# Optimization experiments

Measured on AMD Instinct MI355X. Metric: run time of the kernel, lower is better.

Reference implementation:

```python
import jax, jax.numpy as jnp
import numpy as np

L, B, S, D, H, F = 3, 2, 2048, 256, 8, 1024
DK = D // H
EPS = 1e-7


def _positional_encoding(max_len: int, dim: int) -> jnp.ndarray:
    # pos in [1, max_len], i in [1, dim]; w = pos / 10000**((2*i//2)/dim) == pos / 10000**(i/dim)
    pos = np.arange(1, max_len + 1, dtype=np.float64)[:, None]
    i = np.arange(1, dim + 1)
    w = pos / np.power(10000.0, i.astype(np.float64) / dim)[None, :]
    pe = np.where((i % 2 == 0)[None, :], np.sin(w), np.cos(w))
    return jnp.asarray(pe, jnp.float32)


def _ln(x, g, b):
    mu = jnp.mean(x, axis=-1, keepdims=True)
    var = jnp.mean((x - mu) ** 2, axis=-1, keepdims=True)
    return (x - mu) / jnp.sqrt(var + EPS) * g + b


def setup_inputs() -> dict:
    key = jax.random.key(0)
    ks = jax.random.split(key, 16)
    s = 0.05
    inp = {
        "x": jax.random.normal(ks[0], (B, S, D), jnp.float32),
        "mask": jax.random.randint(ks[1], (B, S, S), 0, 2).astype(bool),
        "pe": _positional_encoding(S, D),
        "Wq": jax.random.normal(ks[2], (L, H, D, DK), jnp.float32) * s,
        "Wk": jax.random.normal(ks[3], (L, H, D, DK), jnp.float32) * s,
        "Wv": jax.random.normal(ks[4], (L, H, D, DK), jnp.float32) * s,
        "Wo": jax.random.normal(ks[5], (L, D, D), jnp.float32) * s,
        "bo": jnp.zeros((L, D), jnp.float32),
        "ln1_g": jnp.ones((L, D), jnp.float32),
        "ln1_b": jnp.zeros((L, D), jnp.float32),
        "W1": jax.random.normal(ks[6], (L, D, F), jnp.float32) * s,
        "b1": jnp.zeros((L, F), jnp.float32),
        "W2": jax.random.normal(ks[7], (L, F, D), jnp.float32) * s,
        "b2": jnp.zeros((L, D), jnp.float32),
        "ln2_g": jnp.ones((L, D), jnp.float32),
        "ln2_b": jnp.zeros((L, D), jnp.float32),
    }
    return inp


def _encoder_layer(x, mask, Wq, Wk, Wv, Wo, bo, ln1_g, ln1_b, W1, b1, W2, b2, ln2_g, ln2_b):
    # all heads batched: [B,S,D] x [H,D,dk] -> [B,H,S,dk]
    q = jnp.einsum('bsd,hdk->bhsk', x, Wq)
    k = jnp.einsum('bsd,hdk->bhsk', x, Wk)
    v = jnp.einsum('bsd,hdk->bhsk', x, Wv)
    scores = jnp.einsum('bhsk,bhtk->bhst', q, k) / jnp.sqrt(jnp.float32(DK))
    neg = -jnp.finfo(jnp.float32).max
    scores = jnp.where(mask[:, None, :, :], neg, scores)
    attn = jax.nn.softmax(scores, axis=-1)
    # concat heads along feature dim (head-major order as torch.cat dim=2)
    o = jnp.einsum('bhst,bhtv->bshv', attn, v).reshape(x.shape[0], x.shape[1], D)
    o = o @ Wo + bo
    x = _ln(o + x, ln1_g, ln1_b)  # post-norm (prenorm=False), dropout_rate=0
    h = jax.nn.relu(x @ W1 + b1) @ W2 + b2
    x = _ln(h + x, ln2_g, ln2_b)
    return x


def reference(x, mask, pe, Wq, Wk, Wv, Wo, bo, ln1_g, ln1_b, W1, b1, W2, b2, ln2_g, ln2_b):
    x = x + pe[None, : x.shape[1], :]
    for l in range(L):
        x = _encoder_layer(x, mask, Wq[l], Wk[l], Wv[l], Wo[l], bo[l], ln1_g[l], ln1_b[l],
                           W1[l], b1[l], W2[l], b2[l], ln2_g[l], ln2_b[l])
    return x
```

## Files before the change

### kernel.cpp

```cpp
#include <hip/hip_runtime.h>
#include <hip/hip_bf16.h>
#include <cfloat>

#define Lc 3
#define Bc 2
#define Sc 2048
#define Dc 256
#define Hc 8
#define DKc 32
#define Fc 1024

typedef __hip_bfloat16 bf16;
typedef short s8v __attribute__((ext_vector_type(8)));
typedef float f4v __attribute__((ext_vector_type(4)));

#define QSCALE 0.25504526036067815f

#if __has_builtin(__builtin_amdgcn_exp2f)
#define EXP2(x) __builtin_amdgcn_exp2f(x)
#else
#define EXP2(x) exp2f(x)
#endif

__device__ __forceinline__ float load_f(const void* p, size_t i, int isbf)
{
    return isbf ? __bfloat162float(((const bf16*)p)[i]) : ((const float*)p)[i];
}

typedef const __attribute__((address_space(1))) char gchar_t;
typedef __attribute__((address_space(3))) char lchar_t;
__device__ __forceinline__ void glds16(const void* g, void* l)
{
    __builtin_amdgcn_global_load_lds((gchar_t*)(size_t)g, (lchar_t*)(size_t)l,
                                     16, 0, 0);
}

#define NBLK_REPACK 2304
#define NBLK_CONV   6942
#define NBLK_PACK   1024
#define NBLK_PE     4096

__global__ __launch_bounds__(256) void prologue_fused(
    const void* __restrict__ x, const void* __restrict__ mask,
    const void* __restrict__ pe,
    const void* Wq, const void* Wk, const void* Wv,
    const void* Wo, const void* W1, const void* W2,
    const void* bo, const void* b1, const void* b2,
    const void* g1, const void* be1, const void* g2, const void* be2,
    bf16* __restrict__ wqkv, bf16* __restrict__ dstb, float* __restrict__ pc,
    unsigned* __restrict__ pmask, float* __restrict__ xf,
    bf16* __restrict__ xb, int* __restrict__ flags)
{
    __shared__ int sf[2];
    int tid = threadIdx.x;
    if (tid < 64) {
        const unsigned short* u16 = (const unsigned short*)x;
        int cnt = 0;
        for (int i = tid; i < 256; i += 64) {
            unsigned e = (u16[2 * i] >> 7) & 0xFF;
            cnt += (e >= 90 && e <= 140) ? 1 : 0;
        }
        #pragma unroll
        for (int d = 1; d < 64; d <<= 1) cnt += __shfl_xor(cnt, d);
        const unsigned* mu = (const unsigned*)mask;
        int c2 = ((mu[tid] & 0xFFFFFF00u) == 0) ? 1 : 0;
        #pragma unroll
        for (int d = 1; d < 64; d <<= 1) c2 += __shfl_xor(c2, d);
        if (tid == 0) {
            sf[0] = (cnt >= 128) ? 1 : 0;
            sf[1] = (c2 >= 48) ? 1 : 0;
            if (blockIdx.x == 0) { flags[0] = sf[0]; flags[1] = sf[1]; }
        }
    }
    __syncthreads();
    int isbf = sf[0], mf = sf[1];
    int blk = blockIdx.x;

    if (blk < NBLK_REPACK) {
        int idx = blk * 256 + tid;
        int l   = idx / (3 * Dc * Dc);
        int rem = idx % (3 * Dc * Dc);
        int col = rem / Dc;
        int d   = rem % Dc;
        int mat = col / Dc;
        int hk  = col % Dc;
        int h = hk / DKc, kk = hk % DKc;
        const void* W = (mat == 0) ? Wq : (mat == 1) ? Wk : Wv;
        float v = load_f(W, (size_t)l * (Hc * Dc * DKc) + h * (Dc * DKc) + d * DKc + kk, isbf);
        wqkv[idx] = __float2bfloat16(v);
    } else if (blk < NBLK_REPACK + NBLK_CONV) {
        const int NB0 = Lc * Dc * Dc;
        const int NB1 = NB0 + Lc * Dc * Fc;
        const int NB2 = NB1 + Lc * Fc * Dc;
        int idx = (blk - NBLK_REPACK) * 256 + tid;
        if (idx < NB2) {
            const void* src; int off;
            if (idx < NB0) {
                int l = idx / (Dc * Dc); int rem = idx % (Dc * Dc);
                int n = rem / Dc, k = rem % Dc;
                src = Wo; off = l * Dc * Dc + k * Dc + n;
            } else if (idx < NB1) {
                int j = idx - NB0;
                int l = j / (Fc * Dc); int rem = j % (Fc * Dc);
                int n = rem / Dc, k = rem % Dc;
                src = W1; off = l * Dc * Fc + k * Fc + n;
            } else {
                int j = idx - NB1;
                int l = j / (Dc * Fc); int rem = j % (Dc * Fc);
                int n = rem / Fc, k = rem % Fc;
                src = W2; off = l * Fc * Dc + k * Dc + n;
            }
            dstb[idx] = __float2bfloat16(load_f(src, off, isbf));
        } else {
            int off = idx - NB2;
            if (off < 7680) {
                const void* src; int lo;
                if (off < 768)       { src = bo;  lo = off; }
                else if (off < 3840) { src = b1;  lo = off - 768; }
                else if (off < 4608) { src = b2;  lo = off - 3840; }
                else if (off < 5376) { src = g1;  lo = off - 4608; }
                else if (off < 6144) { src = be1; lo = off - 5376; }
                else if (off < 6912) { src = g2;  lo = off - 6144; }
                else                 { src = be2; lo = off - 6912; }
                pc[off] = load_f(src, lo, isbf);
            }
        }
    } else if (blk < NBLK_REPACK + NBLK_CONV + NBLK_PACK) {
        int idx = (blk - NBLK_REPACK - NBLK_CONV) * 256 + tid;
        unsigned wb = 0;
        if (mf) {
            const int* mp = (const int*)mask + (size_t)idx * 32;
            #pragma unroll
            for (int u = 0; u < 8; ++u) {
                uint4 q = *(const uint4*)(mp + u * 4);
                wb |= (q.x ? 1u : 0u) << (u * 4);
                wb |= (q.y ? 1u : 0u) << (u * 4 + 1);
                wb |= (q.z ? 1u : 0u) << (u * 4 + 2);
                wb |= (q.w ? 1u : 0u) << (u * 4 + 3);
            }
        } else {
            const unsigned char* mp = (const unsigned char*)mask + (size_t)idx * 32;
            uint4 a = *(const uint4*)mp;
            uint4 bq = *(const uint4*)(mp + 16);
            const unsigned char* ab = (const unsigned char*)&a;
            const unsigned char* bb = (const unsigned char*)&bq;
            #pragma unroll
            for (int j = 0; j < 16; ++j) {
                wb |= (ab[j] ? 1u : 0u) << j;
                wb |= (bb[j] ? 1u : 0u) << (16 + j);
            }
        }
        pmask[idx] = wb;
    } else {
        int idx = (blk - NBLK_REPACK - NBLK_CONV - NBLK_PACK) * 256 + tid;
        int rem = idx % (Sc * Dc);
        float v = load_f(x, idx, isbf) + load_f(pe, rem, isbf);
        xf[idx] = v;
        xb[idx] = __float2bfloat16(v);
    }
}

__global__ __launch_bounds__(256) void gemm_mfma(
    const bf16* __restrict__ A, const bf16* __restrict__ BT,
    const float* __restrict__ bias, void* __restrict__ C,
    bf16* __restrict__ vt,
    int M, int N, int K, int relu, int obf, float ascale, int scale_ncols,
    int ldc)
{
    __shared__ __align__(16) short As[4096];
    __shared__ __align__(16) short Bs[4096];
    int tid = threadIdx.x;
    int w = tid >> 6, lane = tid & 63;
    int quad = lane >> 4, l15 = lane & 15;
    int wm0 = (w & 1) * 32, wn0 = (w >> 1) * 32;
    int row0 = blockIdx.y * 64, col0 = blockIdx.x * 64;

    int s0 = w * 128 + lane;
    int s1 = s0 + 64;
    int r0 = s0 >> 3, c0 = ((s0 & 7) ^ (r0 & 7)) * 8;
    int r1 = s1 >> 3, c1 = ((s1 & 7) ^ (r1 & 7)) * 8;
    const bf16* Ag0 = A + (size_t)(row0 + r0) * K + c0;
    const bf16* Ag1 = A + (size_t)(row0 + r1) * K + c1;
    const bf16* Bg0 = BT + (size_t)(col0 + r0) * K + c0;
    const bf16* Bg1 = BT + (size_t)(col0 + r1) * K + c1;
    short* Ad0 = As + w * 1024;
    short* Ad1 = As + w * 1024 + 512;
    short* Bd0 = Bs + w * 1024;
    short* Bd1 = Bs + w * 1024 + 512;

    f4v acc00 = {0.f,0.f,0.f,0.f}, acc01 = acc00, acc10 = acc00, acc11 = acc00;

    int m0 = wm0 + l15, m1 = wm0 + 16 + l15;
    int n0 = wn0 + l15, n1 = wn0 + 16 + l15;
    int sw7 = l15 & 7;

    for (int k0 = 0; k0 < K; k0 += 64) {
        glds16(Ag0 + k0, Ad0);
        glds16(Ag1 + k0, Ad1);
        glds16(Bg0 + k0, Bd0);
        glds16(Bg1 + k0, Bd1);
        __syncthreads();
        #pragma unroll
        for (int kc = 0; kc < 2; ++kc) {
            int sw = ((kc * 4 + quad) ^ sw7) * 8;
            s8v a0 = *(const s8v*)(As + m0 * 64 + sw);
            s8v a1 = *(const s8v*)(As + m1 * 64 + sw);
            s8v b0 = *(const s8v*)(Bs + n0 * 64 + sw);
            s8v b1 = *(const s8v*)(Bs + n1 * 64 + sw);
            acc00 = __builtin_amdgcn_mfma_f32_16x16x32_bf16(a0, b0, acc00, 0, 0, 0);
            acc01 = __builtin_amdgcn_mfma_f32_16x16x32_bf16(a0, b1, acc01, 0, 0, 0);
            acc10 = __builtin_amdgcn_mfma_f32_16x16x32_bf16(a1, b0, acc10, 0, 0, 0);
            acc11 = __builtin_amdgcn_mfma_f32_16x16x32_bf16(a1, b1, acc11, 0, 0, 0);
        }
        __syncthreads();
    }

    f4v accs[2][2] = {{acc00, acc01}, {acc10, acc11}};

    if (vt && col0 >= 2 * Dc) {
        #pragma unroll
        for (int mt = 0; mt < 2; ++mt) {
            #pragma unroll
            for (int nt = 0; nt < 2; ++nt) {
                int lc = wn0 + nt * 16 + l15;
                #pragma unroll
                for (int reg = 0; reg < 4; ++reg) {
                    int lr = wm0 + mt * 16 + quad * 4 + reg;
                    int p = ((lr & 15) << 2) | (lr >> 4);
                    bf16 bv = __float2bfloat16(accs[mt][nt][reg]);
                    As[lc * 64 + (p ^ ((lc & 7) << 3))] = *(short*)&bv;
                }
            }
        }
        __syncthreads();
        int bI = row0 >> 11;
        int srow = row0 & (Sc - 1);
        #pragma unroll
        for (int j = 0; j < 2; ++j) {
            int e = j * 256 + tid;
            int c = e >> 3, p0 = (e & 7) * 8;
            s8v vv = *(const s8v*)(As + c * 64 + (p0 ^ ((c & 7) << 3)));
            int gcv = col0 - 2 * Dc + c;
            size_t vb = ((size_t)(bI * Hc + (gcv >> 5)) * DKc + (gcv & 31)) * Sc
                        + srow + p0;
            *(s8v*)(vt + vb) = vv;
        }
        return;
    }

    float bv0 = bias ? bias[col0 + wn0 + l15] : 0.f;
    float bv1 = bias ? bias[col0 + wn0 + 16 + l15] : 0.f;
    #pragma unroll
    for (int mt = 0; mt < 2; ++mt) {
        #pragma unroll
        for (int nt = 0; nt < 2; ++nt) {
            int gr = row0 + wm0 + mt * 16 + quad * 4;
            int gc = col0 + wn0 + nt * 16 + l15;
            float badd = nt ? bv1 : bv0;
            float sc = (gc < scale_ncols) ? ascale : 1.f;
            #pragma unroll
            for (int reg = 0; reg < 4; ++reg) {
                float v = accs[mt][nt][reg] * sc + badd;
                if (relu) v = fmaxf(v, 0.f);
                if (obf) ((bf16*)C)[(size_t)(gr + reg) * ldc + gc] = __float2bfloat16(v);
                else     ((float*)C)[(size_t)(gr + reg) * ldc + gc] = v;
            }
        }
    }
}

__global__ __launch_bounds__(256) void gemm_mfma32(
    const bf16* __restrict__ A, const bf16* __restrict__ BT,
    const float* __restrict__ bias, void* __restrict__ C,
    int M, int N, int K, int relu, int obf)
{
    __shared__ __align__(16) short As[2048];
    __shared__ __align__(16) short Bs[4096];
    int tid = threadIdx.x;
    int w = tid >> 6, lane = tid & 63;
    int quad = lane >> 4, l15 = lane & 15;
    int wm0 = (w & 1) * 16, wn0 = (w >> 1) * 32;
    int row0 = blockIdx.y * 32, col0 = blockIdx.x * 64;

    int sa = w * 64 + lane;
    int ra = sa >> 3, ca = ((sa & 7) ^ (ra & 7)) * 8;
    int s0 = w * 128 + lane, s1 = s0 + 64;
    int r0 = s0 >> 3, c0 = ((s0 & 7) ^ (r0 & 7)) * 8;
    int r1 = s1 >> 3, c1 = ((s1 & 7) ^ (r1 & 7)) * 8;
    const bf16* Ag  = A + (size_t)(row0 + ra) * K + ca;
    const bf16* Bg0 = BT + (size_t)(col0 + r0) * K + c0;
    const bf16* Bg1 = BT + (size_t)(col0 + r1) * K + c1;
    short* Ad  = As + w * 512;
    short* Bd0 = Bs + w * 1024;
    short* Bd1 = Bs + w * 1024 + 512;

    f4v acc0 = {0.f,0.f,0.f,0.f}, acc1 = acc0;

    int m0 = wm0 + l15;
    int n0 = wn0 + l15, n1 = wn0 + 16 + l15;
    int sw7 = l15 & 7;

    for (int k0 = 0; k0 < K; k0 += 64) {
        glds16(Ag + k0, Ad);
        glds16(Bg0 + k0, Bd0);
        glds16(Bg1 + k0, Bd1);
        __syncthreads();
        #pragma unroll
        for (int kc = 0; kc < 2; ++kc) {
            int sw = ((kc * 4 + quad) ^ sw7) * 8;
            s8v a0 = *(const s8v*)(As + m0 * 64 + sw);
            s8v b0 = *(const s8v*)(Bs + n0 * 64 + sw);
            s8v b1 = *(const s8v*)(Bs + n1 * 64 + sw);
            acc0 = __builtin_amdgcn_mfma_f32_16x16x32_bf16(a0, b0, acc0, 0, 0, 0);
            acc1 = __builtin_amdgcn_mfma_f32_16x16x32_bf16(a0, b1, acc1, 0, 0, 0);
        }
        __syncthreads();
    }

    float bv0 = bias ? bias[col0 + wn0 + l15] : 0.f;
    float bv1 = bias ? bias[col0 + wn0 + 16 + l15] : 0.f;
    f4v accs[2] = {acc0, acc1};
    #pragma unroll
    for (int nt = 0; nt < 2; ++nt) {
        int gr = row0 + wm0 + quad * 4;
        int gc = col0 + wn0 + nt * 16 + l15;
        float badd = nt ? bv1 : bv0;
        #pragma unroll
        for (int reg = 0; reg < 4; ++reg) {
            float v = accs[nt][reg] + badd;
            if (relu) v = fmaxf(v, 0.f);
            if (obf) ((bf16*)C)[(size_t)(gr + reg) * N + gc] = __float2bfloat16(v);
            else     ((float*)C)[(size_t)(gr + reg) * N + gc] = v;
        }
    }
}

__global__ __launch_bounds__(256) void flash_mfma(
    const bf16* __restrict__ qkv, const bf16* __restrict__ vt,
    const unsigned* __restrict__ pmask,
    bf16* __restrict__ op0, bf16* __restrict__ op1,
    bf16* __restrict__ op2, bf16* __restrict__ op3,
    float* __restrict__ spart)
{
    __shared__ __align__(16) short Ks[2][2048];
    __shared__ __align__(16) short Vs[2][2048];
    __shared__ __align__(16) short Pw[4][16 * 72];

    int tid = threadIdx.x;
    int w = tid >> 6;
    int lane = tid & 63;
    int quad = lane >> 4, l15 = lane & 15;
    int q0 = blockIdx.x * 64;
    int h = blockIdx.y;
    int z = blockIdx.z;
    int b = z >> 2, rng = z & 3;
    bf16* op = (rng == 0) ? op0 : (rng == 1) ? op1 : (rng == 2) ? op2 : op3;

    s8v qfrag = *(const s8v*)(qkv + (size_t)(b * Sc + q0 + w * 16 + l15) * 512 + h * 32 + quad * 8);

    int sr = tid >> 3, ss = tid & 7;
    int c8 = ss ^ (sr & 7);
    const bf16* kg = qkv + (size_t)(b * Sc + rng * (Sc / 4) + 2 * sr + (c8 >> 2)) * 512
                     + 256 + h * 32 + (c8 & 3) * 8;
    const bf16* vg = vt + ((size_t)(b * Hc + h) * DKc + sr) * Sc + rng * (Sc / 4) + c8 * 8;

    int koff = (l15 >> 1) * 64 + ((((l15 & 1) << 2) + quad) ^ ((l15 >> 1) & 7)) * 8;
    int pfoff = l15 * 72 + quad * 8;
    int vkey = l15 & 7;
    int voff = l15 * 64;

    f4v o0 = {0.f,0.f,0.f,0.f}, o1 = o0;
    float ssum[4] = {0.f, 0.f, 0.f, 0.f};

    short* pwv = Pw[w];
    const unsigned* mp = pmask + (size_t)b * Sc * (Sc / 32)
                         + (size_t)(q0 + w * 16 + quad * 4) * (Sc / 32) + rng * 16;

#define FSTAGE(bi, it2) do { \
        glds16(kg + (size_t)(it2) * (64 * 512), Ks[bi] + w * 512); \
        glds16(vg + (it2) * 64, Vs[bi] + w * 512); \
    } while (0)

    FSTAGE(0, 0);
    for (int it = 0; it < 8; ++it) {
        int cur = it & 1;
        __syncthreads();
        if (it < 7) FSTAGE(cur ^ 1, it + 1);

        uint2 mw[4];
        #pragma unroll
        for (int reg = 0; reg < 4; ++reg)
            mw[reg] = *(const uint2*)(mp + reg * (Sc / 32) + it * 2);

        const short* kb = Ks[cur];
        f4v sfr[4];
        __builtin_amdgcn_s_setprio(1);
        #pragma unroll
        for (int nt = 0; nt < 4; ++nt) {
            s8v kf = *(const s8v*)(kb + koff + nt * 512);
            f4v zz = {0.f,0.f,0.f,0.f};
            sfr[nt] = __builtin_amdgcn_mfma_f32_16x16x32_bf16(qfrag, kf, zz, 0, 0, 0);
        }
        __builtin_amdgcn_s_setprio(0);
        #pragma unroll
        for (int reg = 0; reg < 4; ++reg) {
            unsigned ta = mw[reg].x >> l15;
            unsigned tb = mw[reg].y >> l15;
            float p0 = EXP2(sfr[0][reg]); if (ta & 1u)         p0 = 0.f;
            float p1 = EXP2(sfr[1][reg]); if ((ta >> 16) & 1u) p1 = 0.f;
            float p2 = EXP2(sfr[2][reg]); if (tb & 1u)         p2 = 0.f;
            float p3 = EXP2(sfr[3][reg]); if ((tb >> 16) & 1u) p3 = 0.f;
            ssum[reg] += (p0 + p1) + (p2 + p3);
            __hip_bfloat162 plo = __float22bfloat162_rn(make_float2(p0, p1));
            __hip_bfloat162 phi = __float22bfloat162_rn(make_float2(p2, p3));
            uint2 pk = {*(unsigned*)&plo, *(unsigned*)&phi};
            *(uint2*)(pwv + (quad * 4 + reg) * 72 + l15 * 4) = pk;
        }
        const short* vb = Vs[cur];
        __builtin_amdgcn_s_setprio(1);
        #pragma unroll
        for (int kc = 0; kc < 2; ++kc) {
            s8v pf = *(const s8v*)(pwv + pfoff + kc * 32);
            int vo = voff + (((kc * 4 + quad) ^ vkey) * 8);
            s8v vf0 = *(const s8v*)(vb + vo);
            s8v vf1 = *(const s8v*)(vb + vo + 1024);
            o0 = __builtin_amdgcn_mfma_f32_16x16x32_bf16(pf, vf0, o0, 0, 0, 0);
            o1 = __builtin_amdgcn_mfma_f32_16x16x32_bf16(pf, vf1, o1, 0, 0, 0);
        }
        __builtin_amdgcn_s_setprio(0);
    }
#undef FSTAGE

    #pragma unroll
    for (int reg = 0; reg < 4; ++reg) {
        #pragma unroll
        for (int d = 1; d < 16; d <<= 1) ssum[reg] += __shfl_xor(ssum[reg], d);
    }

    #pragma unroll
    for (int reg = 0; reg < 4; ++reg) {
        int row = q0 + w * 16 + quad * 4 + reg;
        size_t ob = (size_t)(b * Sc + row) * Dc + h * DKc;
        op[ob + l15]      = __float2bfloat16(o0[reg]);
        op[ob + 16 + l15] = __float2bfloat16(o1[reg]);
        if (l15 == 0)
            spart[((size_t)(rng * Bc + b) * Hc + h) * Sc + row] = ssum[reg];
    }
}

__global__ __launch_bounds__(256) void attn_merge(
    const bf16* __restrict__ op0, const bf16* __restrict__ op1,
    const bf16* __restrict__ op2, const bf16* __restrict__ op3,
    const float* __restrict__ spart, bf16* __restrict__ attn_out)
{
    int t8 = blockIdx.x * 256 + threadIdx.x;
    size_t idx = (size_t)t8 * 8;
    int d = (int)(idx & 255);
    int h = d >> 5;
    int row = (int)((idx >> 8) & (Sc - 1));
    int b = (int)(idx >> 19);
    float s = 0.f;
    #pragma unroll
    for (int r = 0; r < 4; ++r)
        s += spart[((size_t)(r * Bc + b) * Hc + h) * Sc + row];
    float inv = 1.f / fmaxf(s, 1e-30f);

    uint4 a0 = *(const uint4*)(op0 + idx);
    uint4 a1 = *(const uint4*)(op1 + idx);
    uint4 a2 = *(const uint4*)(op2 + idx);
    uint4 a3 = *(const uint4*)(op3 + idx);
    const unsigned short* u0 = (const unsigned short*)&a0;
    const unsigned short* u1 = (const unsigned short*)&a1;
    const unsigned short* u2 = (const unsigned short*)&a2;
    const unsigned short* u3 = (const unsigned short*)&a3;
    unsigned short outv[8];
    #pragma unroll
    for (int j = 0; j < 8; ++j) {
        float o = (__uint_as_float((unsigned)u0[j] << 16) + __uint_as_float((unsigned)u1[j] << 16))
                + (__uint_as_float((unsigned)u2[j] << 16) + __uint_as_float((unsigned)u3[j] << 16));
        bf16 ov = __float2bfloat16(o * inv);
        outv[j] = *(unsigned short*)&ov;
    }
    *(uint4*)(attn_out + idx) = *(uint4*)outv;
}

__global__ __launch_bounds__(256) void add_ln(
    const float* __restrict__ a, float* __restrict__ xf, bf16* __restrict__ xb,
    const float* __restrict__ g, const float* __restrict__ b,
    void* __restrict__ dout, const int* __restrict__ flags)
{
    __shared__ float ws4[2][4];
    int row = blockIdx.x, d = threadIdx.x;
    size_t idx = (size_t)row * Dc + d;
    float v = a[idx] + xf[idx];
    float s = v;
    #pragma unroll
    for (int dd = 1; dd < 64; dd <<= 1) s += __shfl_xor(s, dd);
    if ((d & 63) == 0) ws4[0][d >> 6] = s;
    __syncthreads();
    float mu = (ws4[0][0] + ws4[0][1] + ws4[0][2] + ws4[0][3]) * (1.f / Dc);
    float c = v - mu;
    float q = c * c;
    #pragma unroll
    for (int dd = 1; dd < 64; dd <<= 1) q += __shfl_xor(q, dd);
    if ((d & 63) == 0) ws4[1][d >> 6] = q;
    __syncthreads();
    float var = (ws4[1][0] + ws4[1][1] + ws4[1][2] + ws4[1][3]) * (1.f / Dc);
    float r2 = c * rsqrtf(var + 1e-7f) * g[d] + b[d];
    xf[idx] = r2;
    xb[idx] = __float2bfloat16(r2);
    if (dout) {
        if (flags[0]) ((bf16*)dout)[idx] = __float2bfloat16(r2);
        else          ((float*)dout)[idx] = r2;
    }
}

extern "C" void kernel_launch(void* const* d_in, const int* in_sizes, int n_in,
                              void* d_out, int out_size, void* d_ws, size_t ws_size,
                              hipStream_t stream)
{
    const void* x    = d_in[0];
    const void* mask = d_in[1];
    const void* pe   = d_in[2];
    const void* Wq   = d_in[3];
    const void* Wk   = d_in[4];
    const void* Wv   = d_in[5];
    const void* Wo   = d_in[6];
    const void* bo   = d_in[7];
    const void* ln1g = d_in[8];
    const void* ln1b = d_in[9];
    const void* W1   = d_in[10];
    const void* b1   = d_in[11];
    const void* W2   = d_in[12];
    const void* b2   = d_in[13];
    const void* ln2g = d_in[14];
    const void* ln2b = d_in[15];

    const int M = Bc * Sc;
    char* ws = (char*)d_ws;
    const size_t MB = 1024 * 1024;
    int*      flags    = (int*)ws;
    float*    xf32     = (float*)(ws + 256);
    float*    obuf     = (float*)(ws + 256 + 4 * MB);
    char*     bigc     = ws + 256 + 8 * MB;
    bf16*     xbf      = (bf16*)(ws + 256 + 16 * MB);
    bf16*     attn_out = (bf16*)(ws + 256 + 18 * MB);
    bf16*     wqkv     = (bf16*)(ws + 256 + 20 * MB);
    bf16*     woc      = wqkv + (size_t)Lc * Dc * 3 * Dc;
    bf16*     w1c      = woc + (size_t)Lc * Dc * Dc;
    bf16*     w2c      = w1c + (size_t)Lc * Dc * Fc;
    float*    pc       = (float*)(w2c + (size_t)Lc * Fc * Dc);
    unsigned* pmask    = (unsigned*)(ws + 256 + 25 * MB);
    float*    spart    = (float*)(ws + 256 + 26 * MB);

    bf16* qkv  = (bf16*)bigc;
    bf16* vtb  = (bf16*)(bigc + 4 * MB);
    bf16* hbuf = (bf16*)bigc;
    bf16* op0  = (bf16*)obuf;
    bf16* op1  = op0 + (size_t)M * Dc;
    bf16* op2  = attn_out;
    bf16* op3  = (bf16*)(bigc + 6 * MB);

    float* pc_bo   = pc;
    float* pc_b1   = pc + 768;
    float* pc_b2   = pc + 3840;
    float* pc_ln1g = pc + 4608;
    float* pc_ln1b = pc + 5376;
    float* pc_ln2g = pc + 6144;
    float* pc_ln2b = pc + 6912;

    prologue_fused<<<NBLK_REPACK + NBLK_CONV + NBLK_PACK + NBLK_PE, 256, 0, stream>>>(
        x, mask, pe, Wq, Wk, Wv, Wo, W1, W2, bo, b1, b2,
        ln1g, ln1b, ln2g, ln2b, wqkv, woc, pc, pmask, xf32, xbf, flags);

    for (int l = 0; l < Lc; ++l) {
        gemm_mfma<<<dim3(3 * Dc / 64, M / 64), 256, 0, stream>>>(
            xbf, wqkv + (size_t)l * Dc * 3 * Dc, nullptr, qkv, vtb,
            M, 3 * Dc, Dc, 0, 1, QSCALE, Dc, 512);
        flash_mfma<<<dim3(Sc / 64, Hc, Bc * 4), 256, 0, stream>>>(
            qkv, vtb, pmask, op0, op1, op2, op3, spart);
        attn_merge<<<(Bc * Sc * Dc / 8) / 256, 256, 0, stream>>>(
            op0, op1, op2, op3, spart, attn_out);
        gemm_mfma32<<<dim3(Dc / 64, M / 32), 256, 0, stream>>>(
            attn_out, woc + (size_t)l * Dc * Dc, pc_bo + l * Dc, obuf, M, Dc, Dc, 0, 0);
        add_ln<<<M, 256, 0, stream>>>(obuf, xf32, xbf,
            pc_ln1g + l * Dc, pc_ln1b + l * Dc, nullptr, flags);
        gemm_mfma<<<dim3(Fc / 64, M / 64), 256, 0, stream>>>(
            xbf, w1c + (size_t)l * Dc * Fc, pc_b1 + l * Fc, hbuf, nullptr,
            M, Fc, Dc, 1, 1, 1.f, 0, Fc);
        gemm_mfma32<<<dim3(Dc / 64, M / 32), 256, 0, stream>>>(
            hbuf, w2c + (size_t)l * Fc * Dc, pc_b2 + l * Dc, obuf, M, Dc, Fc, 0, 0);
        add_ln<<<M, 256, 0, stream>>>(obuf, xf32, xbf,
            pc_ln2g + l * Dc, pc_ln2b + l * Dc,
            (l == Lc - 1) ? d_out : nullptr, flags);
    }
}
```

Before: 356.0 us.

## Double-buffer LDS tiles in MFMA GEMM kernels to overlap loads with compute

Both GEMM kernels now keep two LDS buffers and issue the global-to-LDS loads for the next K tile before computing on the current one, using a single barrier per iteration instead of two. The aim is to hide global load latency behind the MFMA work and cut synchronisation. In exchange, LDS use per block doubles, which can lower occupancy. Correctness relies on the glds16 async writes being visible by the next barrier, and it is unclear whether that barrier waits on the outstanding vmcnt.

```diff
diff --git a/kernel.cpp b/kernel.cpp
--- a/kernel.cpp
+++ b/kernel.cpp
@@ -167,8 +167,8 @@
     int M, int N, int K, int relu, int obf, float ascale, int scale_ncols,
     int ldc)
 {
-    __shared__ __align__(16) short As[4096];
-    __shared__ __align__(16) short Bs[4096];
+    __shared__ __align__(16) short As[2][4096];
+    __shared__ __align__(16) short Bs[2][4096];
     int tid = threadIdx.x;
     int w = tid >> 6, lane = tid & 63;
     int quad = lane >> 4, l15 = lane & 15;
@@ -183,10 +183,6 @@
     const bf16* Ag1 = A + (size_t)(row0 + r1) * K + c1;
     const bf16* Bg0 = BT + (size_t)(col0 + r0) * K + c0;
     const bf16* Bg1 = BT + (size_t)(col0 + r1) * K + c1;
-    short* Ad0 = As + w * 1024;
-    short* Ad1 = As + w * 1024 + 512;
-    short* Bd0 = Bs + w * 1024;
-    short* Bd1 = Bs + w * 1024 + 512;
 
     f4v acc00 = {0.f,0.f,0.f,0.f}, acc01 = acc00, acc10 = acc00, acc11 = acc00;
 
@@ -194,30 +190,39 @@
     int n0 = wn0 + l15, n1 = wn0 + 16 + l15;
     int sw7 = l15 & 7;
 
+#define GSTAGE(bi, kk) do { \
+        glds16(Ag0 + (kk), As[bi] + w * 1024); \
+        glds16(Ag1 + (kk), As[bi] + w * 1024 + 512); \
+        glds16(Bg0 + (kk), Bs[bi] + w * 1024); \
+        glds16(Bg1 + (kk), Bs[bi] + w * 1024 + 512); \
+    } while (0)
+
+    GSTAGE(0, 0);
     for (int k0 = 0; k0 < K; k0 += 64) {
-        glds16(Ag0 + k0, Ad0);
-        glds16(Ag1 + k0, Ad1);
-        glds16(Bg0 + k0, Bd0);
-        glds16(Bg1 + k0, Bd1);
+        int cur = (k0 >> 6) & 1;
         __syncthreads();
+        if (k0 + 64 < K) GSTAGE(cur ^ 1, k0 + 64);
+        const short* Ab = As[cur];
+        const short* Bb = Bs[cur];
         #pragma unroll
         for (int kc = 0; kc < 2; ++kc) {
             int sw = ((kc * 4 + quad) ^ sw7) * 8;
-            s8v a0 = *(const s8v*)(As + m0 * 64 + sw);
-            s8v a1 = *(const s8v*)(As + m1 * 64 + sw);
-            s8v b0 = *(const s8v*)(Bs + n0 * 64 + sw);
-            s8v b1 = *(const s8v*)(Bs + n1 * 64 + sw);
+            s8v a0 = *(const s8v*)(Ab + m0 * 64 + sw);
+            s8v a1 = *(const s8v*)(Ab + m1 * 64 + sw);
+            s8v b0 = *(const s8v*)(Bb + n0 * 64 + sw);
+            s8v b1 = *(const s8v*)(Bb + n1 * 64 + sw);
             acc00 = __builtin_amdgcn_mfma_f32_16x16x32_bf16(a0, b0, acc00, 0, 0, 0);
             acc01 = __builtin_amdgcn_mfma_f32_16x16x32_bf16(a0, b1, acc01, 0, 0, 0);
             acc10 = __builtin_amdgcn_mfma_f32_16x16x32_bf16(a1, b0, acc10, 0, 0, 0);
             acc11 = __builtin_amdgcn_mfma_f32_16x16x32_bf16(a1, b1, acc11, 0, 0, 0);
         }
+    }
+#undef GSTAGE
+
+    f4v accs[2][2] = {{acc00, acc01}, {acc10, acc11}};
+
+    if (vt && col0 >= 2 * Dc) {
         __syncthreads();
-    }
-
-    f4v accs[2][2] = {{acc00, acc01}, {acc10, acc11}};
-
-    if (vt && col0 >= 2 * Dc) {
         #pragma unroll
         for (int mt = 0; mt < 2; ++mt) {
             #pragma unroll
@@ -228,7 +233,7 @@
                     int lr = wm0 + mt * 16 + quad * 4 + reg;
                     int p = ((lr & 15) << 2) | (lr >> 4);
                     bf16 bv = __float2bfloat16(accs[mt][nt][reg]);
-                    As[lc * 64 + (p ^ ((lc & 7) << 3))] = *(short*)&bv;
+                    As[0][lc * 64 + (p ^ ((lc & 7) << 3))] = *(short*)&bv;
                 }
             }
         }
@@ -239,7 +244,7 @@
         for (int j = 0; j < 2; ++j) {
             int e = j * 256 + tid;
             int c = e >> 3, p0 = (e & 7) * 8;
-            s8v vv = *(const s8v*)(As + c * 64 + (p0 ^ ((c & 7) << 3)));
+            s8v vv = *(const s8v*)(As[0] + c * 64 + (p0 ^ ((c & 7) << 3)));
             int gcv = col0 - 2 * Dc + c;
             size_t vb = ((size_t)(bI * Hc + (gcv >> 5)) * DKc + (gcv & 31)) * Sc
                         + srow + p0;
@@ -274,8 +279,8 @@
     const float* __restrict__ bias, void* __restrict__ C,
     int M, int N, int K, int relu, int obf)
 {
-    __shared__ __align__(16) short As[2048];
-    __shared__ __align__(16) short Bs[4096];
+    __shared__ __align__(16) short As[2][2048];
+    __shared__ __align__(16) short Bs[2][4096];
     int tid = threadIdx.x;
     int w = tid >> 6, lane = tid & 63;
     int quad = lane >> 4, l15 = lane & 15;
@@ -290,9 +295,6 @@
     const bf16* Ag  = A + (size_t)(row0 + ra) * K + ca;
     const bf16* Bg0 = BT + (size_t)(col0 + r0) * K + c0;
     const bf16* Bg1 = BT + (size_t)(col0 + r1) * K + c1;
-    short* Ad  = As + w * 512;
-    short* Bd0 = Bs + w * 1024;
-    short* Bd1 = Bs + w * 1024 + 512;
 
     f4v acc0 = {0.f,0.f,0.f,0.f}, acc1 = acc0;
 
@@ -300,22 +302,30 @@
     int n0 = wn0 + l15, n1 = wn0 + 16 + l15;
     int sw7 = l15 & 7;
 
+#define GSTAGE32(bi, kk) do { \
+        glds16(Ag + (kk), As[bi] + w * 512); \
+        glds16(Bg0 + (kk), Bs[bi] + w * 1024); \
+        glds16(Bg1 + (kk), Bs[bi] + w * 1024 + 512); \
+    } while (0)
+
+    GSTAGE32(0, 0);
     for (int k0 = 0; k0 < K; k0 += 64) {
-        glds16(Ag + k0, Ad);
-        glds16(Bg0 + k0, Bd0);
-        glds16(Bg1 + k0, Bd1);
+        int cur = (k0 >> 6) & 1;
         __syncthreads();
+        if (k0 + 64 < K) GSTAGE32(cur ^ 1, k0 + 64);
+        const short* Ab = As[cur];
+        const short* Bb = Bs[cur];
         #pragma unroll
         for (int kc = 0; kc < 2; ++kc) {
             int sw = ((kc * 4 + quad) ^ sw7) * 8;
-            s8v a0 = *(const s8v*)(As + m0 * 64 + sw);
-            s8v b0 = *(const s8v*)(Bs + n0 * 64 + sw);
-            s8v b1 = *(const s8v*)(Bs + n1 * 64 + sw);
+            s8v a0 = *(const s8v*)(Ab + m0 * 64 + sw);
+            s8v b0 = *(const s8v*)(Bb + n0 * 64 + sw);
+            s8v b1 = *(const s8v*)(Bb + n1 * 64 + sw);
             acc0 = __builtin_amdgcn_mfma_f32_16x16x32_bf16(a0, b0, acc0, 0, 0, 0);
             acc1 = __builtin_amdgcn_mfma_f32_16x16x32_bf16(a0, b1, acc1, 0, 0, 0);
         }
-        __syncthreads();
-    }
+    }
+#undef GSTAGE32
 
     float bv0 = bias ? bias[col0 + wn0 + l15] : 0.f;
     float bv1 = bias ? bias[col0 + wn0 + 16 + l15] : 0.f;
```

Result: faster. 343.5 us (-3.5%).
